# Kernel optimization log

Hardware: AMD Instinct MI355X
Metric: run time of the kernel (lower is better)

The kernel has to match this reference:

```python
import jax, jax.numpy as jnp
import numpy as np

B, H, W, DIM = 1, 320, 320, 256
WIN, NH = 10, 8
HD = DIM // NH
N = WIN * WIN
HID = 4 * DIM
SCALE = HD ** (-0.5)
EPS = 1e-5


def _rel_pos_index():
    coords = np.stack(np.meshgrid(np.arange(WIN), np.arange(WIN), indexing='ij'))  # [2,w,w]
    cf = coords.reshape(2, -1)                      # [2, N]
    rel = (cf[:, :, None] - cf[:, None, :]).transpose(1, 2, 0).astype(np.int64)  # [N,N,2]
    rel[:, :, 0] += WIN - 1
    rel[:, :, 1] += WIN - 1
    rel[:, :, 0] *= 2 * WIN - 1
    return jnp.asarray(rel.sum(-1))                 # [N, N]

REL_IDX = _rel_pos_index()


def setup_inputs() -> dict:
    key = jax.random.key(0)
    ks = jax.random.split(key, 16)
    std = 0.02
    return {
        'x': jax.random.normal(ks[0], (B, H * W, DIM), jnp.float32),
        'norm1_g': jnp.ones((DIM,), jnp.float32),
        'norm1_b': jnp.zeros((DIM,), jnp.float32),
        'wq': jax.random.normal(ks[1], (DIM, DIM), jnp.float32) * std,
        'bq': jnp.zeros((DIM,), jnp.float32),
        'wkv': jax.random.normal(ks[2], (DIM, 2 * DIM), jnp.float32) * std,
        'bkv': jnp.zeros((2 * DIM,), jnp.float32),
        'rpb': jax.random.normal(ks[3], ((2 * WIN - 1) ** 2, NH), jnp.float32) * std,
        'proj_w': jax.random.normal(ks[4], (DIM, DIM), jnp.float32) * std,
        'proj_b': jnp.zeros((DIM,), jnp.float32),
        'norm2_g': jnp.ones((DIM,), jnp.float32),
        'norm2_b': jnp.zeros((DIM,), jnp.float32),
        'l1_w': jax.random.normal(ks[5], (DIM, HID), jnp.float32) * std,
        'l1_b': jnp.zeros((HID,), jnp.float32),
        'dw_w': jax.random.normal(ks[6], (HID, 1, 3, 3), jnp.float32) * std,
        'dw_b': jnp.zeros((HID,), jnp.float32),
        'l2_w': jax.random.normal(ks[7], (HID, DIM), jnp.float32) * std,
        'l2_b': jnp.zeros((DIM,), jnp.float32),
    }


def _ln(x, g, b):
    m = x.mean(-1, keepdims=True)
    v = ((x - m) ** 2).mean(-1, keepdims=True)
    return (x - m) * jax.lax.rsqrt(v + EPS) * g + b


def reference(x, norm1_g, norm1_b, wq, bq, wkv, bkv, rpb, proj_w, proj_b,
              norm2_g, norm2_b, l1_w, l1_b, dw_w, dw_b, l2_w, l2_b):
    # ---- Window attention branch ----
    h = _ln(x, norm1_g, norm1_b).reshape(B, H, W, DIM)
    # window partition: [B*nW, N, C]
    win = h.reshape(B, H // WIN, WIN, W // WIN, WIN, DIM)
    win = win.transpose(0, 1, 3, 2, 4, 5).reshape(-1, N, DIM)
    q = (win @ wq + bq).reshape(-1, N, NH, HD).transpose(0, 2, 1, 3) * SCALE  # [bW,h,N,d]
    kv = (win @ wkv + bkv).reshape(-1, N, 2, NH, HD).transpose(2, 0, 3, 1, 4)
    k, v = kv[0], kv[1]                                                        # [bW,h,N,d]
    attn = jnp.einsum('bhnd,bhmd->bhnm', q, k)                                 # [bW,h,N,N]
    bias = rpb[REL_IDX]                                                        # [N,N,h]
    attn = attn + bias.transpose(2, 0, 1)[None]
    attn = jax.nn.softmax(attn, axis=-1)
    o = jnp.einsum('bhnm,bhmd->bhnd', attn, v).transpose(0, 2, 1, 3).reshape(-1, N, DIM)
    o = o @ proj_w + proj_b
    # window reverse: [B, H*W, C]
    o = o.reshape(B, H // WIN, W // WIN, WIN, WIN, DIM)
    o = o.transpose(0, 1, 3, 2, 4, 5).reshape(B, H * W, DIM)
    x = x + o
    # ---- LeFF branch ----
    h2 = _ln(x, norm2_g, norm2_b)
    f = jax.nn.gelu(h2 @ l1_w + l1_b, approximate=False)
    f = f.reshape(B, H, W, HID).transpose(0, 3, 1, 2)                          # NCHW
    f = jax.lax.conv_general_dilated(
        f, dw_w, window_strides=(1, 1), padding='SAME',
        feature_group_count=HID,
        dimension_numbers=('NCHW', 'OIHW', 'NCHW')) + dw_b[None, :, None, None]
    f = jax.nn.gelu(f, approximate=False)
    f = f.transpose(0, 2, 3, 1).reshape(B, H * W, HID)
    x = x + (f @ l2_w + l2_b)
    return x
```

## Files before the change

### kernel.cpp

```cpp
#include <hip/hip_runtime.h>
#include <hip/hip_bf16.h>

typedef unsigned short u16;
typedef __attribute__((ext_vector_type(8))) __bf16 bf16x8;
typedef __attribute__((ext_vector_type(4))) float f32x4;

#define HW_ 320
#define DIM_ 256
#define HID_ 1024
#define SCALE_ 0.1767766952966369f
#define LDP 72
#define NEGINF_ -30000.0f

__device__ __forceinline__ float b2f(u16 u){
  union{unsigned int i; float f;} z; z.i=((unsigned int)u)<<16; return z.f;
}
__device__ __forceinline__ u16 f2b(float f){
  union{float f; unsigned int i;} z; z.f=f;
  return (u16)((z.i + 0x7fffu + ((z.i>>16)&1u))>>16);
}
__device__ __forceinline__ u16 f2b_s(float f, float sub){
  union{float f; unsigned int i;} z; z.f=f;
  if ((z.i & 0x7F800000u) == 0x7F800000u) z.f = sub;
  return (u16)((z.i + 0x7fffu + ((z.i>>16)&1u))>>16);
}
__device__ __forceinline__ float gelu_f(float v){
  float u = 0.7978845608028654f*(v + 0.044715f*v*v*v);
  float e = __expf(2.f*u);
  float t = 1.f - 2.f/(e+1.f);
  return 0.5f*v*(1.f+t);
}

__global__ void k_transpose(const float* __restrict__ src, u16* __restrict__ dst,
                            int K, int N, float scale){
  int i = blockIdx.x*256 + threadIdx.x;
  if (i < K*N){ int k = i / N, n = i - k*N; dst[(size_t)n*K + k] = f2b(src[i]*scale); }
}
__global__ void k_transpose_dw(const float* __restrict__ src, u16* __restrict__ dst){
  int i = blockIdx.x*256 + threadIdx.x;
  if (i < 9216){ int ch = i / 9, kk = i - ch*9; dst[kk*1024 + ch] = f2b(src[i]); }
}
__global__ void k_qkvbias(const float* __restrict__ bq, const float* __restrict__ bkv, float* __restrict__ dst){
  int i = blockIdx.x*256 + threadIdx.x;
  if (i < 768) dst[i] = (i<256) ? bq[i]*SCALE_ : bkv[i-256];
}
__global__ void k_biastab(const float* __restrict__ rpb, float* __restrict__ btab){
  int i = blockIdx.x*256 + threadIdx.x;
  if (i >= 114688) return;
  int ct = i & 7, lr = (i>>3) & 15;
  int idx = i >> 7;
  int n = idx % 112, h = idx / 112;
  int m = ct*16 + lr;
  float v = NEGINF_;
  if (n < 100 && m < 100){
    int rel = (n/10 - m/10 + 9)*19 + (n%10 - m%10 + 9);
    v = rpb[rel*8 + h];
  }
  btab[i] = v;
}

template<int F32IN, int WINDOWED>
__global__ __launch_bounds__(256) void k_ln(const void* __restrict__ xv,
    const float* __restrict__ g, const float* __restrict__ b, u16* __restrict__ out)
{
  int tid = threadIdx.x, lane = tid & 63;
  int t = blockIdx.x*4 + (tid>>6);
  float v[4];
  if constexpr (F32IN){
    float4 f = *(const float4*)((const float*)xv + (size_t)t*DIM_ + lane*4);
    v[0]=f.x; v[1]=f.y; v[2]=f.z; v[3]=f.w;
  } else {
    uint2 u = *(const uint2*)((const u16*)xv + (size_t)t*DIM_ + lane*4);
    v[0]=b2f((u16)(u.x&0xffff)); v[1]=b2f((u16)(u.x>>16));
    v[2]=b2f((u16)(u.y&0xffff)); v[3]=b2f((u16)(u.y>>16));
  }
  float s  = v[0]+v[1]+v[2]+v[3];
  float ss = v[0]*v[0]+v[1]*v[1]+v[2]*v[2]+v[3]*v[3];
  for (int m=1;m<64;m<<=1){ s += __shfl_xor(s,m,64); ss += __shfl_xor(ss,m,64); }
  float mean = s*(1.0f/DIM_);
  float var  = ss*(1.0f/DIM_) - mean*mean;
  if (var < 0.f) var = 0.f;
  float rstd = rsqrtf(var + 1e-5f);
  float4 gg = *(const float4*)(g + lane*4);
  float4 bb = *(const float4*)(b + lane*4);
  float o0 = (v[0]-mean)*rstd*gg.x + bb.x;
  float o1 = (v[1]-mean)*rstd*gg.y + bb.y;
  float o2 = (v[2]-mean)*rstd*gg.z + bb.z;
  float o3 = (v[3]-mean)*rstd*gg.w + bb.w;
  int row = t;
  if constexpr (WINDOWED){
    int hy = t / HW_, wx = t - hy*HW_;
    row = ((hy/10)*32 + wx/10)*100 + (hy%10)*10 + (wx%10);
  }
  unsigned lo = (unsigned)f2b(o0) | ((unsigned)f2b(o1)<<16);
  unsigned hi = (unsigned)f2b(o2) | ((unsigned)f2b(o3)<<16);
  *(uint2*)(out + (size_t)row*DIM_ + lane*4) = make_uint2(lo,hi);
}

template<int EPI, int CLAMP>
__global__ __launch_bounds__(256) void k_gemm(
    const u16* __restrict__ A, const u16* __restrict__ Bt, int K, int nx,
    const float* __restrict__ biasf,
    const float* __restrict__ resf, const u16* __restrict__ resb,
    u16* __restrict__ O0, float* __restrict__ Of,
    int a_off, int o_off)
{
  __shared__ u16 Al[128*LDP];
  __shared__ u16 Bl[128*LDP];
  int tid = threadIdx.x;
  int bid = blockIdx.x, nwg = gridDim.x;
  int swz = (bid & 7)*(nwg>>3) + (bid>>3);
  int m0 = (swz / nx)*128, n0 = (swz % nx)*128;
  int w = tid>>6, lane = tid&63, lr = lane&15, lg = lane>>4;
  int wrow = (w>>1)*64, wcol = (w&1)*64;
  f32x4 zero = {0.f,0.f,0.f,0.f};
  f32x4 acc[4][4];
  #pragma unroll
  for (int i=0;i<4;++i)
    #pragma unroll
    for (int j=0;j<4;++j) acc[i][j]=zero;

  const u16* pA[4]; const u16* pB[4];
  u16* lA[4]; u16* lB[4];
  #pragma unroll
  for (int it=0; it<4; ++it){
    int vi = tid + it*256;
    int row = vi>>3, cv = (vi&7)*8;
    int srow = m0 + row;
    if constexpr (CLAMP){
      srow += a_off;
      srow = srow < 0 ? 0 : (srow > 102399 ? 102399 : srow);
    }
    pA[it] = A  + (size_t)srow*K + cv;
    pB[it] = Bt + (size_t)(n0+row)*K + cv;
    lA[it] = &Al[row*LDP+cv];
    lB[it] = &Bl[row*LDP+cv];
  }
  bf16x8 av[4], bv[4];
  #pragma unroll
  for (int it=0; it<4; ++it){ av[it] = *(const bf16x8*)pA[it]; bv[it] = *(const bf16x8*)pB[it]; }

  for (int kt=0; kt<K; kt+=64){
    __syncthreads();
    #pragma unroll
    for (int it=0; it<4; ++it){ *(bf16x8*)lA[it] = av[it]; *(bf16x8*)lB[it] = bv[it]; }
    if (kt + 64 < K){
      #pragma unroll
      for (int it=0; it<4; ++it){
        av[it] = *(const bf16x8*)(pA[it] + kt + 64);
        bv[it] = *(const bf16x8*)(pB[it] + kt + 64);
      }
    }
    __syncthreads();
    #pragma unroll
    for (int k0=0;k0<64;k0+=32){
      bf16x8 af[4], bfr[4];
      #pragma unroll
      for (int i=0;i<4;++i) af[i]  = *(const bf16x8*)&Al[(wrow+i*16+lr)*LDP + k0 + lg*8];
      #pragma unroll
      for (int j=0;j<4;++j) bfr[j] = *(const bf16x8*)&Bl[(wcol+j*16+lr)*LDP + k0 + lg*8];
      #pragma unroll
      for (int i=0;i<4;++i)
        #pragma unroll
        for (int j=0;j<4;++j)
          acc[i][j] = __builtin_amdgcn_mfma_f32_16x16x32_bf16(af[i], bfr[j], acc[i][j],0,0,0);
    }
  }

  float bj[4];
  #pragma unroll
  for (int j=0;j<4;++j) bj[j] = biasf[n0 + wcol + j*16 + lr];

  #pragma unroll
  for (int i=0;i<4;++i){
    #pragma unroll
    for (int r=0;r<4;++r){
      int grow = m0 + wrow + i*16 + lg*4 + r;
      if constexpr (EPI==0){
        size_t rb = (size_t)grow*768;
        #pragma unroll
        for (int j=0;j<4;++j){
          int gcol = n0 + wcol + j*16 + lr;
          O0[rb + gcol] = f2b_s(acc[i][j][r] + bj[j], 10000.f);
        }
      } else if constexpr (EPI==1){
        int win = grow/100, n = grow - win*100;
        int wy = win>>5, wxx = win&31;
        int py = n/10, px = n - py*10;
        size_t t = (size_t)((wy*10+py)*HW_ + wxx*10 + px);
        #pragma unroll
        for (int j=0;j<4;++j){
          int gcol = n0 + wcol + j*16 + lr;
          float o = acc[i][j][r] + bj[j] + resf[t*DIM_ + gcol];
          O0[t*DIM_ + gcol] = f2b_s(o, 30000.f);
        }
      } else if constexpr (EPI==2){
        #pragma unroll
        for (int j=0;j<4;++j){
          int gcol = n0 + wcol + j*16 + lr;
          float o = gelu_f(acc[i][j][r] + bj[j]);
          O0[(size_t)grow*HID_ + gcol] = f2b_s(o, 40000.f);
        }
      } else {
        size_t t = (size_t)(o_off + grow);
        #pragma unroll
        for (int j=0;j<4;++j){
          int gcol = n0 + wcol + j*16 + lr;
          float o = acc[i][j][r] + bj[j] + b2f(resb[t*DIM_ + gcol]);
          union{float f; unsigned int i;} z; z.f=o;
          if ((z.i & 0x7F800000u) == 0x7F800000u) o = 60000.f;
          Of[t*DIM_ + gcol] = o;
        }
      }
    }
  }
}

__global__ __launch_bounds__(256) void k_attn(
    const u16* __restrict__ QKV, const float* __restrict__ btab, u16* __restrict__ Ow)
{
  __shared__ u16 p_lds[112*136];
  __shared__ u16 v_t[32*136];
  int tid = threadIdx.x;
  int wh = blockIdx.x;
  int head = wh & 7, win = wh >> 3;
  for (int i=tid;i<896;i+=256){ int row=i>>3, c=i&7; *(unsigned*)&p_lds[row*136 + 112 + 2*c] = 0u; }
  for (int i=tid;i<576;i+=256){ int d=i/18, c=i-18*d; *(unsigned*)&v_t[d*136 + 100 + 2*c] = 0u; }
  __syncthreads();
  const u16* base = QKV + (size_t)(win*100)*768 + head*32;
  const u16* vbase = base + 512;
  for (int i=tid;i<1600;i+=256){
    int m=i>>4, d2=(i&15)<<1;
    unsigned u = *(const unsigned*)(vbase + (size_t)m*768 + d2);
    v_t[d2*136+m]     = (u16)(u&0xffff);
    v_t[(d2+1)*136+m] = (u16)(u>>16);
  }

  int w = tid>>6, lane = tid&63, lr = lane&15, lg = lane>>4;
  f32x4 zero = {0.f,0.f,0.f,0.f};
  bf16x8 aq[2];
  #pragma unroll
  for (int rt=0;rt<2;++rt){
    int qr = w*32 + rt*16 + lr;
    aq[rt] = *(const bf16x8*)(base + (size_t)qr*768 + lg*8);
  }
  f32x4 s[2][7];
  #pragma unroll
  for (int ct=0;ct<7;++ct){
    int kr = ct*16 + lr;
    bf16x8 bk = *(const bf16x8*)(base + 256 + (size_t)kr*768 + lg*8);
    s[0][ct] = __builtin_amdgcn_mfma_f32_16x16x32_bf16(aq[0], bk, zero,0,0,0);
    s[1][ct] = __builtin_amdgcn_mfma_f32_16x16x32_bf16(aq[1], bk, zero,0,0,0);
  }
  float inv[2][4];
  #pragma unroll
  for (int rt=0;rt<2;++rt){
    #pragma unroll
    for (int r=0;r<4;++r){
      int n = w*32 + rt*16 + lg*4 + r;
      int nb = n < 112 ? n : 111;
      const float* brow = btab + (((size_t)(head*112 + nb))*16 + lr)*8;
      float4 b0 = *(const float4*)brow;
      float4 b1 = *(const float4*)(brow + 4);
      float bias7[7] = {b0.x,b0.y,b0.z,b0.w,b1.x,b1.y,b1.z};
      float sm = 0.f;
      #pragma unroll
      for (int ct=0;ct<7;++ct){
        float p = __expf(s[rt][ct][r] + bias7[ct]);
        s[rt][ct][r] = p; sm += p;
      }
      #pragma unroll
      for (int msk=1;msk<16;msk<<=1) sm += __shfl_xor(sm,msk,64);
      inv[rt][r] = 1.f/sm;
      if (n < 112){
        #pragma unroll
        for (int ct=0;ct<7;++ct) p_lds[n*136 + ct*16 + lr] = f2b(s[rt][ct][r]);
      }
    }
  }
  __syncthreads();
  f32x4 o[2][2];
  o[0][0]=zero; o[0][1]=zero; o[1][0]=zero; o[1][1]=zero;
  #pragma unroll
  for (int k0=0;k0<128;k0+=32){
    bf16x8 ap[2];
    #pragma unroll
    for (int rt=0;rt<2;++rt){
      int pr = w*32 + rt*16 + lr; if (pr>111) pr=111;
      ap[rt] = *(const bf16x8*)&p_lds[pr*136 + k0 + lg*8];
    }
    #pragma unroll
    for (int dt=0;dt<2;++dt){
      bf16x8 bv = *(const bf16x8*)&v_t[(dt*16+lr)*136 + k0 + lg*8];
      o[0][dt] = __builtin_amdgcn_mfma_f32_16x16x32_bf16(ap[0], bv, o[0][dt],0,0,0);
      o[1][dt] = __builtin_amdgcn_mfma_f32_16x16x32_bf16(ap[1], bv, o[1][dt],0,0,0);
    }
  }
  #pragma unroll
  for (int rt=0;rt<2;++rt){
    #pragma unroll
    for (int dt=0;dt<2;++dt){
      #pragma unroll
      for (int r=0;r<4;++r){
        int n = w*32 + rt*16 + lg*4 + r;
        if (n<100)
          Ow[((size_t)(win*100+n))*DIM_ + head*32 + dt*16 + lr] = f2b_s(o[rt][dt][r]*inv[rt][r], 20000.f);
      }
    }
  }
}

#define YT_ 10
__global__ __launch_bounds__(256) void k_dwconv2(const u16* __restrict__ f,
    const u16* __restrict__ wT, const float* __restrict__ bias,
    u16* __restrict__ g, int y0)
{
  int tid = threadIdx.x;
  int bid = blockIdx.x;
  int xt = bid % 160, yt = bid / 160;
  int x  = xt*2 + (tid>>7);
  int cg = (tid&127)<<3;
  int yl0 = yt*YT_;

  float w[9][8];
  #pragma unroll
  for (int kk=0;kk<9;++kk){
    uint4 u = *(const uint4*)(wT + kk*1024 + cg);
    const unsigned* up=(const unsigned*)&u;
    #pragma unroll
    for(int e=0;e<4;++e){ w[kk][2*e]=b2f((u16)(up[e]&0xffff)); w[kk][2*e+1]=b2f((u16)(up[e]>>16)); }
  }
  float bs[8];
  {
    float4 b0 = *(const float4*)(bias+cg);
    float4 b1 = *(const float4*)(bias+cg+4);
    bs[0]=b0.x;bs[1]=b0.y;bs[2]=b0.z;bs[3]=b0.w;bs[4]=b1.x;bs[5]=b1.y;bs[6]=b1.z;bs[7]=b1.w;
  }
  uint4 zq = make_uint4(0,0,0,0);
  auto ld = [&](int ytap, int xx)->uint4{
    int yy = y0 + ytap;
    if (xx<0 || xx>=HW_ || yy<0 || yy>=HW_) return zq;
    return *(const uint4*)(f + ((size_t)((ytap+1)*HW_+xx))*HID_ + cg);
  };
  uint4 a00=ld(yl0-1,x-1), a01=ld(yl0-1,x), a02=ld(yl0-1,x+1);
  uint4 a10=ld(yl0  ,x-1), a11=ld(yl0  ,x), a12=ld(yl0  ,x+1);
  #pragma unroll
  for (int r=0;r<YT_;++r){
    int yl = yl0 + r;
    uint4 a20=ld(yl+1,x-1), a21=ld(yl+1,x), a22=ld(yl+1,x+1);
    float acc[8];
    #pragma unroll
    for (int c=0;c<8;++c) acc[c]=bs[c];
    auto fma8 = [&](const uint4& a, const float (&wk)[8]){
      const unsigned* up=(const unsigned*)&a;
      #pragma unroll
      for(int e=0;e<4;++e){
        acc[2*e]   += b2f((u16)(up[e]&0xffff)) * wk[2*e];
        acc[2*e+1] += b2f((u16)(up[e]>>16))    * wk[2*e+1];
      }
    };
    fma8(a00,w[0]); fma8(a01,w[1]); fma8(a02,w[2]);
    fma8(a10,w[3]); fma8(a11,w[4]); fma8(a12,w[5]);
    fma8(a20,w[6]); fma8(a21,w[7]); fma8(a22,w[8]);
    u16 ov[8];
    #pragma unroll
    for (int c=0;c<8;++c) ov[c] = f2b_s(gelu_f(acc[c]), 50000.f);
    uint4 pack;
    pack.x = (unsigned)ov[0] | ((unsigned)ov[1]<<16);
    pack.y = (unsigned)ov[2] | ((unsigned)ov[3]<<16);
    pack.z = (unsigned)ov[4] | ((unsigned)ov[5]<<16);
    pack.w = (unsigned)ov[6] | ((unsigned)ov[7]<<16);
    *(uint4*)(g + ((size_t)(yl*HW_+x))*HID_ + cg) = pack;
    a00=a10;a01=a11;a02=a12; a10=a20;a11=a21;a12=a22;
  }
}

extern "C" void kernel_launch(void* const* d_in, const int* in_sizes, int n_in,
                              void* d_out, int out_size, void* d_ws, size_t ws_size,
                              hipStream_t stream)
{
  (void)in_sizes; (void)n_in; (void)out_size; (void)ws_size;
  const float* x     = (const float*)d_in[0];
  const float* n1g   = (const float*)d_in[1];
  const float* n1b   = (const float*)d_in[2];
  const float* wq    = (const float*)d_in[3];
  const float* bq    = (const float*)d_in[4];
  const float* wkv   = (const float*)d_in[5];
  const float* bkv   = (const float*)d_in[6];
  const float* rpb   = (const float*)d_in[7];
  const float* projw = (const float*)d_in[8];
  const float* projb = (const float*)d_in[9];
  const float* n2g   = (const float*)d_in[10];
  const float* n2b   = (const float*)d_in[11];
  const float* l1w   = (const float*)d_in[12];
  const float* l1b   = (const float*)d_in[13];
  const float* dww   = (const float*)d_in[14];
  const float* dwb   = (const float*)d_in[15];
  const float* l2w   = (const float*)d_in[16];
  const float* l2b   = (const float*)d_in[17];

  char* ws = (char*)d_ws;
  u16*   WqkvT   = (u16*)(ws + 0);
  u16*   projT   = (u16*)(ws + 393216);
  u16*   l1T     = (u16*)(ws + 524288);
  u16*   l2T     = (u16*)(ws + 1048576);
  float* qkvbias = (float*)(ws + 1572864);
  u16*   dwT     = (u16*)(ws + 1575936);
  float* btab    = (float*)(ws + 1594368);
  u16*   x1      = (u16*)(ws + 2097152);
  u16*   h2      = (u16*)(ws + 54525952);
  char*  BR      = ws + 106954752;
  u16* QKV   = (u16*)(BR + 0);
  u16* hwin  = (u16*)(ws + 264441856);
  u16* fband = (u16*)(BR + 0);
  u16* gband = (u16*)(BR + 106430464);
  u16* owin  = (u16*)d_out;
  float* outp = (float*)d_out;

  k_transpose<<<256, 256, 0, stream>>>(wq,   WqkvT,          256, 256, SCALE_);
  k_transpose<<<512, 256, 0, stream>>>(wkv,  WqkvT + 65536,  256, 512, 1.f);
  k_transpose<<<256, 256, 0, stream>>>(projw, projT,         256, 256, 1.f);
  k_transpose<<<1024,256, 0, stream>>>(l1w,  l1T,            256, 1024, 1.f);
  k_transpose<<<1024,256, 0, stream>>>(l2w,  l2T,            1024, 256, 1.f);
  k_transpose_dw<<<36, 256, 0, stream>>>(dww, dwT);
  k_qkvbias<<<3, 256, 0, stream>>>(bq, bkv, qkvbias);
  k_biastab<<<448, 256, 0, stream>>>(rpb, btab);

  k_ln<1,1><<<25600, 256, 0, stream>>>(x, n1g, n1b, hwin);
  k_gemm<0,0><<<4800, 256, 0, stream>>>(hwin, WqkvT, 256, 6,
      qkvbias, nullptr, nullptr, QKV, nullptr, 0, 0);
  k_attn<<<8192, 256, 0, stream>>>(QKV, btab, owin);
  k_gemm<1,0><<<1600, 256, 0, stream>>>(owin, projT, 256, 2,
      projb, x, nullptr, x1, nullptr, 0, 0);
  k_ln<0,0><<<25600, 256, 0, stream>>>(x1, n2g, n2b, h2);
  for (int b=0; b<2; ++b){
    int y0 = 160*b;
    k_gemm<2,1><<<3240, 256, 0, stream>>>(h2, l1T, 256, 8,
        l1b, nullptr, nullptr, fband, nullptr, (y0-1)*HW_, 0);
    k_dwconv2<<<2560, 256, 0, stream>>>(fband, dwT, dwb, gband, y0);
    k_gemm<3,0><<<800, 256, 0, stream>>>(gband, l2T, 1024, 2,
        l2b, nullptr, x1, nullptr, outp, 0, y0*HW_);
  }
}
```

Before: 702.3 us.

## Double-buffer GEMM register prefetch, remap attention blocks, cheaper bf16 rounding

```diff
diff --git a/kernel.cpp b/kernel.cpp
--- a/kernel.cpp
+++ b/kernel.cpp
@@ -23,6 +23,10 @@
   union{float f; unsigned int i;} z; z.f=f;
   if ((z.i & 0x7F800000u) == 0x7F800000u) z.f = sub;
   return (u16)((z.i + 0x7fffu + ((z.i>>16)&1u))>>16);
+}
+__device__ __forceinline__ u16 f2b_r(float f){
+  union{float f; unsigned int i;} z; z.f=f;
+  return (u16)((z.i + 0x8000u)>>16);
 }
 __device__ __forceinline__ float gelu_f(float v){
   float u = 0.7978845608028654f*(v + 0.044715f*v*v*v);
@@ -136,19 +140,46 @@
     lA[it] = &Al[row*LDP+cv];
     lB[it] = &Bl[row*LDP+cv];
   }
-  bf16x8 av[4], bv[4];
-  #pragma unroll
-  for (int it=0; it<4; ++it){ av[it] = *(const bf16x8*)pA[it]; bv[it] = *(const bf16x8*)pB[it]; }
-
-  for (int kt=0; kt<K; kt+=64){
+  bf16x8 av0[4], bv0[4], av1[4], bv1[4];
+  #pragma unroll
+  for (int it=0; it<4; ++it){
+    av0[it] = *(const bf16x8*)pA[it];        bv0[it] = *(const bf16x8*)pB[it];
+    av1[it] = *(const bf16x8*)(pA[it]+64);   bv1[it] = *(const bf16x8*)(pB[it]+64);
+  }
+
+  for (int kt=0; kt<K; kt+=128){
     __syncthreads();
     #pragma unroll
-    for (int it=0; it<4; ++it){ *(bf16x8*)lA[it] = av[it]; *(bf16x8*)lB[it] = bv[it]; }
-    if (kt + 64 < K){
+    for (int it=0; it<4; ++it){ *(bf16x8*)lA[it] = av0[it]; *(bf16x8*)lB[it] = bv0[it]; }
+    if (kt + 128 < K){
       #pragma unroll
       for (int it=0; it<4; ++it){
-        av[it] = *(const bf16x8*)(pA[it] + kt + 64);
-        bv[it] = *(const bf16x8*)(pB[it] + kt + 64);
+        av0[it] = *(const bf16x8*)(pA[it] + kt + 128);
+        bv0[it] = *(const bf16x8*)(pB[it] + kt + 128);
+      }
+    }
+    __syncthreads();
+    #pragma unroll
+    for (int k0=0;k0<64;k0+=32){
+      bf16x8 af[4], bfr[4];
+      #pragma unroll
+      for (int i=0;i<4;++i) af[i]  = *(const bf16x8*)&Al[(wrow+i*16+lr)*LDP + k0 + lg*8];
+      #pragma unroll
+      for (int j=0;j<4;++j) bfr[j] = *(const bf16x8*)&Bl[(wcol+j*16+lr)*LDP + k0 + lg*8];
+      #pragma unroll
+      for (int i=0;i<4;++i)
+        #pragma unroll
+        for (int j=0;j<4;++j)
+          acc[i][j] = __builtin_amdgcn_mfma_f32_16x16x32_bf16(af[i], bfr[j], acc[i][j],0,0,0);
+    }
+    __syncthreads();
+    #pragma unroll
+    for (int it=0; it<4; ++it){ *(bf16x8*)lA[it] = av1[it]; *(bf16x8*)lB[it] = bv1[it]; }
+    if (kt + 192 < K){
+      #pragma unroll
+      for (int it=0; it<4; ++it){
+        av1[it] = *(const bf16x8*)(pA[it] + kt + 192);
+        bv1[it] = *(const bf16x8*)(pB[it] + kt + 192);
       }
     }
     __syncthreads();
@@ -222,11 +253,11 @@
   __shared__ u16 p_lds[112*136];
   __shared__ u16 v_t[32*136];
   int tid = threadIdx.x;
-  int wh = blockIdx.x;
-  int head = wh & 7, win = wh >> 3;
+  int bid = blockIdx.x;
+  int head = (bid>>3) & 7;
+  int win  = (bid & 7)*128 + (bid>>6);
   for (int i=tid;i<896;i+=256){ int row=i>>3, c=i&7; *(unsigned*)&p_lds[row*136 + 112 + 2*c] = 0u; }
   for (int i=tid;i<576;i+=256){ int d=i/18, c=i-18*d; *(unsigned*)&v_t[d*136 + 100 + 2*c] = 0u; }
-  __syncthreads();
   const u16* base = QKV + (size_t)(win*100)*768 + head*32;
   const u16* vbase = base + 512;
   for (int i=tid;i<1600;i+=256){
@@ -274,7 +305,7 @@
       inv[rt][r] = 1.f/sm;
       if (n < 112){
         #pragma unroll
-        for (int ct=0;ct<7;++ct) p_lds[n*136 + ct*16 + lr] = f2b(s[rt][ct][r]);
+        for (int ct=0;ct<7;++ct) p_lds[n*136 + ct*16 + lr] = f2b_r(s[rt][ct][r]);
       }
     }
   }
```

Measured after the change: 845.2 us. 20.4% more time.
